# Performance work log

Measured on AMD Instinct MI355X. Metric: run time of the kernel, lower is better.

The kernel has to match this reference:

```python
import jax, jax.numpy as jnp
import numpy as np

EPS = 8.0 / 255.0  # hparams['epsilon']


def setup_inputs() -> dict:
    key = jax.random.key(0)
    k1, k2, k3, k4 = jax.random.split(key, 4)
    B, N, C, H, Wd, K = 128, 96, 3, 32, 32, 10
    D = C * H * Wd
    imgs = jax.random.uniform(k1, (B, C, H, Wd), dtype=jnp.float32)
    # sample_deltas: uniform in [-eps, eps]
    deltas = 2.0 * EPS * jax.random.uniform(k2, (N, B, C, H, Wd), dtype=jnp.float32) - EPS
    W = jax.random.normal(k3, (D, K), dtype=jnp.float32) * (1.0 / np.sqrt(D))
    b = jnp.zeros((K,), dtype=jnp.float32)
    labels = jax.random.randint(k4, (B,), 0, K, dtype=jnp.int32)
    ind = 91  # math.ceil(N * proportion) - 1 with N=96, proportion=0.95
    return {"imgs": imgs, "deltas": deltas, "W": W, "b": b, "labels": labels, "ind": ind}


def reference(imgs, deltas, W, b, labels, ind):
    N, B = deltas.shape[:2]
    # pert_imgs = clamp(imgs + delta, 0, 1), flattened for the linear classifier
    x = jnp.clip(imgs[None] + deltas, 0.0, 1.0).reshape(N, B, -1)  # [N,B,D]
    logits = jnp.einsum('nbd,dk->nbk', x, W) + b                    # [N,B,K]
    logp = jax.nn.log_softmax(logits, axis=-1)
    # pert_loss1 = CE(logits, labels), per-sample
    loss1 = -jnp.take_along_axis(logp, labels[None, :, None], axis=-1)[..., 0]  # [N,B]
    # top-2 labels; new_labels = second-best class
    _, top2 = jax.lax.top_k(logits, 2)
    top1, second = top2[..., 0], top2[..., 1]
    loss2 = -jnp.take_along_axis(logp, second[..., None], axis=-1)[..., 0]      # [N,B]
    # mask: if argmax != label, pert_loss2[i] = -10000
    loss2 = jnp.where(top1 == labels[None, :], loss2, jnp.float32(-10000.0))
    # layout [B,N] as in torch.cat(..., dim=1)
    l1 = loss1.T
    l2 = loss2.T
    order = jnp.argsort(l1 - l2, axis=1)                 # sort(loss1 - loss2) indices
    sel_idx = order[:, ind]                              # per-sample selected column
    # torch.tensor(list) detaches -> no gradient through selected losses
    selected = jax.lax.stop_gradient(jnp.take_along_axis(l2, sel_idx[:, None], axis=1))  # [B,1]
    robust_loss = jnp.mean(jnp.mean(l1 - selected, axis=1))
    return robust_loss
```

## Files before the change

### kernel.cpp

```cpp
#include <hip/hip_runtime.h>
#include <hip/hip_bf16.h>
#include <math.h>

#define BB 128
#define NN 96
#define DD 3072
#define KK 10
#define SPL 8
#define KST 12

typedef short s16x8 __attribute__((ext_vector_type(8)));
typedef float f32x4 __attribute__((ext_vector_type(4)));

__global__ __launch_bounds__(256) void k0_pack(
    const float* __restrict__ W, unsigned short* __restrict__ pwg)
{
    const int r = blockIdx.x * 256 + threadIdx.x;
    const int col  = r & 15;
    const int quad = (r >> 4) & 3;
    const int kb   = r >> 6;
    union { unsigned short us[8]; uint4 v; } rec;
#pragma unroll
    for (int j = 0; j < 8; ++j) {
        const int k = kb * 32 + quad * 8 + j;
        const float v = (col < KK) ? W[k * KK + col] : 0.0f;
        const __hip_bfloat16 h = __float2bfloat16(v);
        __builtin_memcpy(&rec.us[j], &h, 2);
    }
    ((uint4*)pwg)[r] = rec.v;
}

__global__ __launch_bounds__(512) void k1_mfma(
    const float* __restrict__ imgs,
    const float* __restrict__ deltas,
    const unsigned short* __restrict__ pwg,
    const float* __restrict__ bias,
    const int*   __restrict__ labels,
    float* __restrict__ l1_ws,
    float* __restrict__ l2_ws)
{
    const int lane = threadIdx.x & 63;
    const int wv   = threadIdx.x >> 6;
    const int tile = blockIdx.x;
    const int r0   = tile * 16;
    const int n    = r0 >> 7;
    const int b0   = r0 & 127;
    const int m    = lane & 15;
    const int quad = lane >> 4;

    const float* ap = deltas + (size_t)(r0 + m) * DD + wv * (KST * 32) + quad * 8;
    const float* ip = imgs   + (size_t)(b0 + m) * DD + wv * (KST * 32) + quad * 8;
    const unsigned short* wp = pwg + ((size_t)(wv * KST) * 64 + lane) * 8;

    f32x4 acc = {0.f, 0.f, 0.f, 0.f};
#pragma unroll 2
    for (int s = 0; s < KST; ++s) {
        const float4 d0 = *(const float4*)(ap);
        const float4 d1 = *(const float4*)(ap + 4);
        const float4 i0 = *(const float4*)(ip);
        const float4 i1 = *(const float4*)(ip + 4);
        const s16x8 bfrag = *(const s16x8*)(wp);
        float x[8];
        x[0] = d0.x + i0.x; x[1] = d0.y + i0.y; x[2] = d0.z + i0.z; x[3] = d0.w + i0.w;
        x[4] = d1.x + i1.x; x[5] = d1.y + i1.y; x[6] = d1.z + i1.z; x[7] = d1.w + i1.w;
        s16x8 afrag;
#pragma unroll
        for (int j = 0; j < 8; ++j) {
            const float xc = fminf(fmaxf(x[j], 0.f), 1.f);
            const __hip_bfloat16 h = __float2bfloat16(xc);
            unsigned short us; __builtin_memcpy(&us, &h, 2);
            afrag[j] = (short)us;
        }
        acc = __builtin_amdgcn_mfma_f32_16x16x32_bf16(afrag, bfrag, acc, 0, 0, 0);
        ap += 32; ip += 32; wp += 512;
    }

    __shared__ float sred[SPL][16][16];
#pragma unroll
    for (int reg = 0; reg < 4; ++reg)
        sred[wv][quad * 4 + reg][m] = acc[reg];
    __syncthreads();

    if (wv == 0 && lane < 16) {
        const int rr = lane;
        float lg[KK];
#pragma unroll
        for (int k = 0; k < KK; ++k) {
            float s = 0.f;
#pragma unroll
            for (int sp = 0; sp < SPL; ++sp) s += sred[sp][rr][k];
            lg[k] = s + bias[k];
        }
        int top1 = 0; float m1 = lg[0];
#pragma unroll
        for (int k = 1; k < KK; ++k) if (lg[k] > m1) { m1 = lg[k]; top1 = k; }
        int sec = (top1 == 0) ? 1 : 0; float m2 = lg[sec];
#pragma unroll
        for (int k = 0; k < KK; ++k)
            if (k != top1 && lg[k] > m2) { m2 = lg[k]; sec = k; }
        float se = 0.f;
#pragma unroll
        for (int k = 0; k < KK; ++k) se += expf(lg[k] - m1);
        const float lse = m1 + logf(se);
        const int b = b0 + rr;
        const int lab = labels[b];
        const float loss1 = lse - lg[lab];
        const float loss2 = (top1 == lab) ? (lse - lg[sec]) : -10000.0f;
        l1_ws[b * NN + n] = loss1;
        l2_ws[b * NN + n] = loss2;
    }
}

__global__ __launch_bounds__(128) void k2_select(
    const float* __restrict__ l1_ws, const float* __restrict__ l2_ws,
    const int* __restrict__ ind_p, float* __restrict__ perb)
{
    const int b = blockIdx.x;
    const int t = threadIdx.x;
    __shared__ float sd[NN];
    __shared__ float sl2[NN];
    __shared__ float ssel;
    __shared__ float swsum[2];

    float myl1 = 0.f, myd = 0.f;
    if (t < NN) {
        const float a = l1_ws[b * NN + t];
        const float c = l2_ws[b * NN + t];
        myl1 = a; myd = a - c;
        sd[t] = myd; sl2[t] = c;
    }
    __syncthreads();

    if (t < NN) {
        int rank = 0;
        for (int j = 0; j < NN; ++j) {
            const float dj = sd[j];
            rank += (dj < myd) || (dj == myd && j < t);
        }
        if (rank == ind_p[0]) ssel = sl2[t];
    }

    float s = myl1;
#pragma unroll
    for (int off = 32; off >= 1; off >>= 1) s += __shfl_down(s, off, 64);
    if ((t & 63) == 0) swsum[t >> 6] = s;
    __syncthreads();
    if (t == 0) {
        const float total = swsum[0] + swsum[1];
        perb[b] = total / 96.0f - ssel;
    }
}

__global__ __launch_bounds__(128) void k3_final(
    const float* __restrict__ perb, float* __restrict__ out)
{
    const int t = threadIdx.x;
    float s = perb[t];
#pragma unroll
    for (int off = 32; off >= 1; off >>= 1) s += __shfl_down(s, off, 64);
    __shared__ float sw[2];
    if ((t & 63) == 0) sw[t >> 6] = s;
    __syncthreads();
    if (t == 0) out[0] = (sw[0] + sw[1]) / 128.0f;
}

extern "C" void kernel_launch(void* const* d_in, const int* in_sizes, int n_in,
                              void* d_out, int out_size, void* d_ws, size_t ws_size,
                              hipStream_t stream) {
    const float* imgs   = (const float*)d_in[0];
    const float* deltas = (const float*)d_in[1];
    const float* W      = (const float*)d_in[2];
    const float* bias   = (const float*)d_in[3];
    const int*   labels = (const int*)d_in[4];
    const int*   ind    = (const int*)d_in[5];
    float* out = (float*)d_out;

    float* l1_ws = (float*)d_ws;
    float* l2_ws = l1_ws + NN * BB;
    float* perb  = l2_ws + NN * BB;
    unsigned short* pwg = (unsigned short*)(perb + BB);

    k0_pack<<<dim3(24), dim3(256), 0, stream>>>(W, pwg);
    k1_mfma<<<dim3(768), dim3(512), 0, stream>>>(
        imgs, deltas, pwg, bias, labels, l1_ws, l2_ws);
    k2_select<<<dim3(BB), dim3(128), 0, stream>>>(l1_ws, l2_ws, ind, perb);
    k3_final<<<dim3(1), dim3(128), 0, stream>>>(perb, out);
}
```

Baseline: 238.8 us.

## Remap MFMA tiles to share one image per block and merge selection kernels

Each MFMA block now covers 16 perturbation samples of the same image instead of 16 images of one sample, so every block reads a single image row. The per-image selection kernel and the final reduction kernel are merged into one 1024-thread single-block kernel. It stages all losses in about 96 KB of LDS, ranks them and reduces straight to the output. This removes a kernel launch and the intermediate per-image buffer, but the ranking work that used to be spread over 128 blocks now runs on one block.

Result: slower. 270.2 us (+13.2%).

```diff
diff --git a/kernel.cpp b/kernel.cpp
--- a/kernel.cpp
+++ b/kernel.cpp
@@ -42,14 +42,13 @@
     const int lane = threadIdx.x & 63;
     const int wv   = threadIdx.x >> 6;
     const int tile = blockIdx.x;
-    const int r0   = tile * 16;
-    const int n    = r0 >> 7;
-    const int b0   = r0 & 127;
+    const int b    = tile & 127;
+    const int n0   = (tile >> 7) * 16;
     const int m    = lane & 15;
     const int quad = lane >> 4;
 
-    const float* ap = deltas + (size_t)(r0 + m) * DD + wv * (KST * 32) + quad * 8;
-    const float* ip = imgs   + (size_t)(b0 + m) * DD + wv * (KST * 32) + quad * 8;
+    const float* ap = deltas + ((size_t)(n0 + m) * BB + b) * DD + wv * (KST * 32) + quad * 8;
+    const float* ip = imgs   + (size_t)b * DD + wv * (KST * 32) + quad * 8;
     const unsigned short* wp = pwg + ((size_t)(wv * KST) * 64 + lane) * 8;
 
     f32x4 acc = {0.f, 0.f, 0.f, 0.f};
@@ -102,66 +101,67 @@
 #pragma unroll
         for (int k = 0; k < KK; ++k) se += expf(lg[k] - m1);
         const float lse = m1 + logf(se);
-        const int b = b0 + rr;
         const int lab = labels[b];
         const float loss1 = lse - lg[lab];
         const float loss2 = (top1 == lab) ? (lse - lg[sec]) : -10000.0f;
+        const int n = n0 + rr;
         l1_ws[b * NN + n] = loss1;
         l2_ws[b * NN + n] = loss2;
     }
 }
 
-__global__ __launch_bounds__(128) void k2_select(
+__global__ __launch_bounds__(1024) void k2_final(
     const float* __restrict__ l1_ws, const float* __restrict__ l2_ws,
-    const int* __restrict__ ind_p, float* __restrict__ perb)
+    const int* __restrict__ ind_p, float* __restrict__ out)
 {
-    const int b = blockIdx.x;
     const int t = threadIdx.x;
-    __shared__ float sd[NN];
-    __shared__ float sl2[NN];
-    __shared__ float ssel;
-    __shared__ float swsum[2];
+    __shared__ float sdiff[BB * NN];
+    __shared__ float sl2[BB * NN];
+    __shared__ float ssel[BB];
+    __shared__ float wpart[16];
 
-    float myl1 = 0.f, myd = 0.f;
-    if (t < NN) {
-        const float a = l1_ws[b * NN + t];
-        const float c = l2_ws[b * NN + t];
-        myl1 = a; myd = a - c;
-        sd[t] = myd; sl2[t] = c;
+    float suml1 = 0.f;
+#pragma unroll
+    for (int r = 0; r < 12; ++r) {
+        const int p = t + r * 1024;
+        const float a = l1_ws[p];
+        const float c = l2_ws[p];
+        suml1 += a;
+        sdiff[p] = a - c;
+        sl2[p]   = c;
     }
     __syncthreads();
 
-    if (t < NN) {
+    const int ind = ind_p[0];
+#pragma unroll
+    for (int r = 0; r < 12; ++r) {
+        const int p = t + r * 1024;
+        const int b = p / NN;
+        const int n = p - b * NN;
+        const float d = sdiff[p];
         int rank = 0;
+        const float* row = sdiff + b * NN;
         for (int j = 0; j < NN; ++j) {
-            const float dj = sd[j];
-            rank += (dj < myd) || (dj == myd && j < t);
+            const float dj = row[j];
+            rank += (dj < d) || (dj == d && j < n);
         }
-        if (rank == ind_p[0]) ssel = sl2[t];
+        if (rank == ind) ssel[b] = sl2[p];
     }
 
-    float s = myl1;
 #pragma unroll
-    for (int off = 32; off >= 1; off >>= 1) s += __shfl_down(s, off, 64);
-    if ((t & 63) == 0) swsum[t >> 6] = s;
+    for (int off = 32; off >= 1; off >>= 1) suml1 += __shfl_down(suml1, off, 64);
+    if ((t & 63) == 0) wpart[t >> 6] = suml1;
     __syncthreads();
-    if (t == 0) {
-        const float total = swsum[0] + swsum[1];
-        perb[b] = total / 96.0f - ssel;
+    if (t < 64) {
+        float s  = (t < 16) ? wpart[t] : 0.f;
+#pragma unroll
+        for (int off = 8; off >= 1; off >>= 1) s += __shfl_down(s, off, 64);
+        float se = ssel[t] + ssel[t + 64];
+#pragma unroll
+        for (int off = 32; off >= 1; off >>= 1) se += __shfl_down(se, off, 64);
+        if (t == 0)
+            out[0] = s / (96.0f * 128.0f) - se / 128.0f;
     }
-}
-
-__global__ __launch_bounds__(128) void k3_final(
-    const float* __restrict__ perb, float* __restrict__ out)
-{
-    const int t = threadIdx.x;
-    float s = perb[t];
-#pragma unroll
-    for (int off = 32; off >= 1; off >>= 1) s += __shfl_down(s, off, 64);
-    __shared__ float sw[2];
-    if ((t & 63) == 0) sw[t >> 6] = s;
-    __syncthreads();
-    if (t == 0) out[0] = (sw[0] + sw[1]) / 128.0f;
 }
 
 extern "C" void kernel_launch(void* const* d_in, const int* in_sizes, int n_in,
@@ -177,12 +177,10 @@
 
     float* l1_ws = (float*)d_ws;
     float* l2_ws = l1_ws + NN * BB;
-    float* perb  = l2_ws + NN * BB;
-    unsigned short* pwg = (unsigned short*)(perb + BB);
+    unsigned short* pwg = (unsigned short*)(l2_ws + NN * BB);
 
     k0_pack<<<dim3(24), dim3(256), 0, stream>>>(W, pwg);
     k1_mfma<<<dim3(768), dim3(512), 0, stream>>>(
         imgs, deltas, pwg, bias, labels, l1_ws, l2_ws);
-    k2_select<<<dim3(BB), dim3(128), 0, stream>>>(l1_ws, l2_ws, ind, perb);
-    k3_final<<<dim3(1), dim3(128), 0, stream>>>(perb, out);
+    k2_final<<<dim3(1), dim3(1024), 0, stream>>>(l1_ws, l2_ws, ind, out);
 }
```
